# Performance work log

Measured on AMD Instinct MI355X. Metric: run time of the kernel, lower is better.

The kernel has to match this reference:

```python
import jax, jax.numpy as jnp
import numpy as np

EPS = 1e-5
TEMP = 2.0

def _dwconv(x, k, dil):
    # depthwise conv, NCHW, kernel OIHW with I=1, groups=C, 'same' padding
    p = dil
    return jax.lax.conv_general_dilated(
        x, k, window_strides=(1, 1), padding=[(p, p), (p, p)],
        rhs_dilation=(dil, dil),
        dimension_numbers=('NCHW', 'OIHW', 'NCHW'),
        feature_group_count=x.shape[1])

def _bn_gelu(y, g, b, m, v):
    scale = (g / jnp.sqrt(v + EPS))[None, :, None, None]
    z = (y - m[None, :, None, None]) * scale + b[None, :, None, None]
    return jax.nn.gelu(z, approximate=False)  # torch nn.GELU default = exact erf

def _pw(feat, w, b):
    # 1x1 pointwise conv with bias
    return jnp.einsum('oi,bihw->bohw', w, feat) + b[None, :, None, None]

def _forward(x, rw, rb,
             e0_k, e0_g, e0_b, e0_m, e0_v, e0_pw, e0_pb,
             e1_k, e1_g, e1_b, e1_m, e1_v, e1_pw, e1_pb,
             e2_k, e2_g, e2_b, e2_m, e2_v, e2_pw, e2_pb):
    # ---- global routing (eval mode: no noise) ----
    pooled = x.mean(axis=(2, 3))                    # [B, C]
    logits = pooled @ rw.T + rb                     # [B, 3]
    prob = jax.nn.softmax(logits / TEMP, axis=-1)
    tp, ti = jax.lax.top_k(prob, 1)                 # top_k = 1
    w = (tp / tp.sum(axis=-1, keepdims=True))[:, 0] # [B], == 1.0 for k=1
    idx = ti[:, 0]                                  # [B]

    # ---- heterogeneous experts, each over full batch, masked by weight ----
    f0 = _pw(_bn_gelu(_dwconv(x, e0_k, 1), e0_g, e0_b, e0_m, e0_v), e0_pw, e0_pb)
    f1 = _pw(_bn_gelu(_dwconv(x, e1_k, 2), e1_g, e1_b, e1_m, e1_v), e1_pw, e1_pb)
    f2 = _pw(_bn_gelu(jnp.einsum('oi,bihw->bohw', e2_k, x), e2_g, e2_b, e2_m, e2_v), e2_pw, e2_pb)

    out = jnp.zeros_like(x)
    for i, fi in enumerate((f0, f1, f2)):
        wi = jnp.where(idx == i, w, 0.0)[:, None, None, None]
        out = out + wi * fi
    return out

def setup_inputs() -> dict:
    key = jax.random.key(0)
    ks = jax.random.split(key, 24)
    B, C, H, W = 32, 256, 64, 64
    d = {
        'x': jax.random.normal(ks[0], (B, C, H, W), jnp.float32),
        'rw': jax.random.normal(ks[1], (3, C), jnp.float32) * 0.02,
        'rb': jnp.zeros((3,), jnp.float32),
    }
    kshapes = [(C, 1, 3, 3), (C, 1, 3, 3), (C, C)]
    for i in range(3):
        base = 2 + i * 4
        d[f'e{i}_k'] = jax.random.normal(ks[base], kshapes[i], jnp.float32) * 0.1
        d[f'e{i}_g'] = jnp.ones((C,), jnp.float32)
        d[f'e{i}_b'] = jnp.zeros((C,), jnp.float32)
        d[f'e{i}_m'] = jax.random.normal(ks[base + 1], (C,), jnp.float32) * 0.1
        d[f'e{i}_v'] = jax.random.uniform(ks[base + 2], (C,), jnp.float32, 0.5, 1.5)
        d[f'e{i}_pw'] = jax.random.normal(ks[base + 3], (C, C), jnp.float32) / np.sqrt(C)
        d[f'e{i}_pb'] = jnp.zeros((C,), jnp.float32)
    return d

def reference(x, rw, rb,
              e0_k, e0_g, e0_b, e0_m, e0_v, e0_pw, e0_pb,
              e1_k, e1_g, e1_b, e1_m, e1_v, e1_pw, e1_pb,
              e2_k, e2_g, e2_b, e2_m, e2_v, e2_pw, e2_pb):
    return _forward(x, rw, rb,
                    e0_k, e0_g, e0_b, e0_m, e0_v, e0_pw, e0_pb,
                    e1_k, e1_g, e1_b, e1_m, e1_v, e1_pw, e1_pb,
                    e2_k, e2_g, e2_b, e2_m, e2_v, e2_pw, e2_pb)
```

## Files before the change

kernel.cpp:

```cpp
#include <hip/hip_runtime.h>
#include <math.h>

#define C 256
#define H 64
#define W 64
#define B 32
#define HW (H*W)
#define EPS 1e-5f
#define LSTR2 256

typedef __attribute__((ext_vector_type(8))) short short8;
typedef __attribute__((ext_vector_type(4))) short short4v;
typedef __attribute__((ext_vector_type(4))) float f32x4;

__device__ __forceinline__ float gelu_exact(float z) {
    return 0.5f * z * (1.0f + erff(z * 0.70710678f));
}
__device__ __forceinline__ short f2bf(float f) {
    union { float f; unsigned u; } v; v.f = f;
    unsigned r = v.u + 0x7fffu + ((v.u >> 16) & 1u);
    return (short)(r >> 16);
}
__device__ __forceinline__ float bf2f(short s) {
    union { unsigned u; float f; } v; v.u = ((unsigned)(unsigned short)s) << 16;
    return v.f;
}
__device__ __forceinline__ int swz8(int w) {
    return (((w & 7) ^ ((w >> 3) & 7)) << 3);
}
__device__ __forceinline__ void swz_hb(int bx, int by, int& h, int& b) {
    int wg  = bx + (by << 6);
    int xcd = wg & 7, lin = wg >> 3;
    b = lin >> 3;
    int j = lin & 7;
    h = (((xcd + b) & 7) << 3) + j;
}

__global__ __launch_bounds__(256) void pool_kernel(const float* __restrict__ x,
                                                   float* __restrict__ pooled) {
    int bc = blockIdx.x;
    const float4* p4 = (const float4*)(x + (size_t)bc * HW);
    int t = threadIdx.x;
    float s = 0.f;
    for (int i = t; i < HW/4; i += 256) {
        float4 v = p4[i];
        s += v.x + v.y + v.z + v.w;
    }
    for (int off = 32; off > 0; off >>= 1) s += __shfl_down(s, off, 64);
    __shared__ float wsum[4];
    if ((t & 63) == 0) wsum[t >> 6] = s;
    __syncthreads();
    if (t == 0) pooled[bc] = (wsum[0]+wsum[1]+wsum[2]+wsum[3]) * (1.f/HW);
}

__global__ __launch_bounds__(256) void prep_kernel(
    const float* __restrict__ s0, const float* __restrict__ s1,
    const float* __restrict__ s2, const float* __restrict__ s3,
    const float* __restrict__ e0k, const float* __restrict__ e1k,
    const float* __restrict__ g0, const float* __restrict__ b0,
    const float* __restrict__ m0, const float* __restrict__ v0,
    const float* __restrict__ g1, const float* __restrict__ b1,
    const float* __restrict__ m1, const float* __restrict__ v1,
    const float* __restrict__ g2, const float* __restrict__ b2,
    const float* __restrict__ m2, const float* __restrict__ v2,
    const float* __restrict__ pooled, const float* __restrict__ rw,
    const float* __restrict__ rb, int* __restrict__ idx,
    short* __restrict__ apackAll, float* __restrict__ kf0, float* __restrict__ kf1,
    float* __restrict__ scAll, float* __restrict__ shAll)
{
    if (blockIdx.x < 192) {
        int gid = blockIdx.x * 256 + threadIdx.x;
        int mat = gid >> 13;
        int c   = gid & 8191;
        int lane = c & 63;
        int ktmt = c >> 6;
        int mt = ktmt & 15, kt = ktmt >> 4;
        int o  = mt*16 + (lane & 15);
        int ci = kt*32 + (lane >> 4)*8;
        const float* src = (mat == 0) ? s0 : (mat == 1) ? s1 :
                           (mat == 2 || mat == 4) ? s2 : s3;
        bool lo = (mat >= 4);
        const float* p = src + o*C + ci;
        short8 v;
#pragma unroll
        for (int j = 0; j < 8; ++j) {
            float f = p[j];
            short hj = f2bf(f);
            v[j] = lo ? f2bf(f - bf2f(hj)) : hj;
        }
        *(short8*)&apackAll[(size_t)gid * 8] = v;
    } else if (blockIdx.x == 192) {
        int t = threadIdx.x;
        {
            float s = g0[t] / sqrtf(v0[t] + EPS);
            scAll[t] = s; shAll[t] = b0[t] - m0[t]*s;
#pragma unroll
            for (int j = 0; j < 9; ++j) kf0[t*12+j] = e0k[t*9+j]*s;
            kf0[t*12+9] = 0.f; kf0[t*12+10] = 0.f; kf0[t*12+11] = 0.f;
        }
        {
            float s = g1[t] / sqrtf(v1[t] + EPS);
            scAll[C+t] = s; shAll[C+t] = b1[t] - m1[t]*s;
#pragma unroll
            for (int j = 0; j < 9; ++j) kf1[t*12+j] = e1k[t*9+j]*s;
            kf1[t*12+9] = 0.f; kf1[t*12+10] = 0.f; kf1[t*12+11] = 0.f;
        }
        {
            float s = g2[t] / sqrtf(v2[t] + EPS);
            scAll[2*C+t] = s; shAll[2*C+t] = b2[t] - m2[t]*s;
        }
    } else {
        int t = threadIdx.x;
        if (t < 192) {
            int e = t >> 6, lane = t & 63;
            __shared__ float lg[3*B];
            for (int b = 0; b < B; ++b) {
                const float* p = pooled + b*C;
                const float* w = rw + e*C;
                float s = 0.f;
#pragma unroll
                for (int i = 0; i < 4; ++i) s += p[lane + i*64] * w[lane + i*64];
                for (int off = 32; off > 0; off >>= 1) s += __shfl_down(s, off, 64);
                if (lane == 0) lg[b*3 + e] = s + rb[e];
            }
            __syncthreads();
            if (t < B) {
                float l0 = lg[t*3], l1 = lg[t*3+1], l2 = lg[t*3+2];
                int best = 0; float bv = l0;
                if (l1 > bv) { bv = l1; best = 1; }
                if (l2 > bv) { bv = l2; best = 2; }
                idx[t] = best;
            }
        } else {
            __syncthreads();
        }
    }
}

template<int DIL>
__device__ __forceinline__ void conv_rows_t(const float* __restrict__ x,
                                            const float* __restrict__ kf,
                                            const float* __restrict__ sh,
                                            short* __restrict__ lds,
                                            int b, int h, int t) {
    const int strip = t & 7;
    const int w0 = strip * 8;
    const int cib = t >> 3;
#pragma unroll 1
    for (int iter = 0; iter < 8; ++iter) {
        int ci = iter*32 + cib;
        const float* xpl = x + (size_t)(b*C + ci) * HW;
        float fr[3][16];
        bool rv[3];
#pragma unroll
        for (int ky = 0; ky < 3; ++ky) {
            int y = h + (ky - 1)*DIL;
            rv[ky] = ((unsigned)y < H);
            if (rv[ky]) {
                const float* row = xpl + y*W;
                float4 fa = (strip > 0) ? *(const float4*)(row + w0 - 4) : float4{0,0,0,0};
                float4 fb = *(const float4*)(row + w0);
                float4 fc = *(const float4*)(row + w0 + 4);
                float4 fd = (strip < 7) ? *(const float4*)(row + w0 + 8) : float4{0,0,0,0};
                fr[ky][0]=fa.x; fr[ky][1]=fa.y; fr[ky][2]=fa.z; fr[ky][3]=fa.w;
                fr[ky][4]=fb.x; fr[ky][5]=fb.y; fr[ky][6]=fb.z; fr[ky][7]=fb.w;
                fr[ky][8]=fc.x; fr[ky][9]=fc.y; fr[ky][10]=fc.z; fr[ky][11]=fc.w;
                fr[ky][12]=fd.x; fr[ky][13]=fd.y; fr[ky][14]=fd.z; fr[ky][15]=fd.w;
            }
        }
        float4 k0 = *(const float4*)(kf + ci*12);
        float4 k1v = *(const float4*)(kf + ci*12 + 4);
        float wk[9] = {k0.x,k0.y,k0.z,k0.w,k1v.x,k1v.y,k1v.z,k1v.w, kf[ci*12+8]};
        float acc8[8] = {0,0,0,0,0,0,0,0};
#pragma unroll
        for (int ky = 0; ky < 3; ++ky) {
            if (rv[ky]) {
#pragma unroll
                for (int kx = 0; kx < 3; ++kx) {
                    float wv = wk[ky*3+kx];
                    const int base = 4 + (kx - 1)*DIL;
#pragma unroll
                    for (int j = 0; j < 8; ++j) acc8[j] += wv * fr[ky][base + j];
                }
            }
        }
        float shv = sh[ci];
#pragma unroll
        for (int j = 0; j < 8; ++j) {
            int w = w0 + j;
            lds[w*LSTR2 + (ci ^ swz8(w))] = f2bf(gelu_exact(acc8[j] + shv));
        }
    }
}

__global__ __launch_bounds__(256) void kconv(
    const float* __restrict__ x, const int* __restrict__ idx,
    const float* __restrict__ kf0, const float* __restrict__ kf1,
    const float* __restrict__ shAll, const short* __restrict__ apackAll,
    const float* __restrict__ e0pb, const float* __restrict__ e1pb,
    float* __restrict__ out)
{
    __shared__ short lds[W*LSTR2];
    int h, b;
    swz_hb(blockIdx.x, blockIdx.y, h, b);
    const int e = idx[b];
    if (e >= 2) return;
    const int t = threadIdx.x;
    const int lane = t & 63, wid = t >> 6;
    const int l15 = lane & 15, quad = lane >> 4;

    if (e == 0) conv_rows_t<1>(x, kf0, shAll,     lds, b, h, t);
    else        conv_rows_t<2>(x, kf1, shAll + C, lds, b, h, t);
    __syncthreads();

    const short* pwf = apackAll + (size_t)e * 65536;
    f32x4 acc[4][4];
#pragma unroll
    for (int i = 0; i < 4; ++i)
#pragma unroll
        for (int wt = 0; wt < 4; ++wt) acc[i][wt] = (f32x4){0.f,0.f,0.f,0.f};
    for (int kt = 0; kt < 8; ++kt) {
        short8 bf[4];
#pragma unroll
        for (int wt = 0; wt < 4; ++wt) {
            int w = wt*16 + l15;
            bf[wt] = *(const short8*)&lds[w*LSTR2 + ((kt*32 + quad*8) ^ swz8(w))];
        }
        short8 af[4];
#pragma unroll
        for (int i = 0; i < 4; ++i)
            af[i] = *(const short8*)&pwf[((size_t)(kt*16 + wid*4 + i)*64 + lane)*8];
#pragma unroll
        for (int i = 0; i < 4; ++i)
#pragma unroll
            for (int wt = 0; wt < 4; ++wt)
                acc[i][wt] = __builtin_amdgcn_mfma_f32_16x16x32_bf16(
                    af[i], bf[wt], acc[i][wt], 0, 0, 0);
    }

    const float* pb = (e == 0) ? e0pb : e1pb;
#pragma unroll
    for (int i = 0; i < 4; ++i) {
        int ob = wid*64 + i*16 + quad*4;
        float4 p4 = *(const float4*)&pb[ob];
        float pbv[4] = {p4.x, p4.y, p4.z, p4.w};
#pragma unroll
        for (int wt = 0; wt < 4; ++wt) {
            int w = wt*16 + l15;
#pragma unroll
            for (int r = 0; r < 4; ++r)
                out[((size_t)(b*C + ob + r))*HW + h*W + w] = acc[i][wt][r] + pbv[r];
        }
    }
}

__device__ __forceinline__ void gemm3t(const short* __restrict__ aH,
                                       const short* __restrict__ aL,
                                       const short* __restrict__ ldsH,
                                       const short* __restrict__ ldsL,
                                       int lane, int wid, f32x4 acc[4][4])
{
    const int l15 = lane & 15, quad = lane >> 4;
    for (int kt = 0; kt < 8; ++kt) {
        short8 bH[4], bL[4];
#pragma unroll
        for (int wt = 0; wt < 4; ++wt) {
            int w = wt*16 + l15;
            int off = w*LSTR2 + ((kt*32 + quad*8) ^ swz8(w));
            bH[wt] = *(const short8*)&ldsH[off];
            bL[wt] = *(const short8*)&ldsL[off];
        }
        short8 fH[4], fL[4];
#pragma unroll
        for (int i = 0; i < 4; ++i) {
            size_t off = ((size_t)(kt*16 + wid*4 + i)*64 + lane)*8;
            fH[i] = *(const short8*)&aH[off];
            fL[i] = *(const short8*)&aL[off];
        }
#pragma unroll
        for (int i = 0; i < 4; ++i)
#pragma unroll
            for (int wt = 0; wt < 4; ++wt) {
                acc[i][wt] = __builtin_amdgcn_mfma_f32_16x16x32_bf16(fH[i], bH[wt], acc[i][wt], 0, 0, 0);
                acc[i][wt] = __builtin_amdgcn_mfma_f32_16x16x32_bf16(fH[i], bL[wt], acc[i][wt], 0, 0, 0);
                acc[i][wt] = __builtin_amdgcn_mfma_f32_16x16x32_bf16(fL[i], bH[wt], acc[i][wt], 0, 0, 0);
            }
    }
}

__global__ __launch_bounds__(256) void ke2(
    const float* __restrict__ x, const int* __restrict__ idx,
    const float* __restrict__ scAll, const float* __restrict__ shAll,
    const short* __restrict__ apackAll, const float* __restrict__ e2pb,
    float* __restrict__ out)
{
    __shared__ short ldsH[W*LSTR2];
    __shared__ short ldsL[W*LSTR2];
    int h, b;
    swz_hb(blockIdx.x, blockIdx.y, h, b);
    if (idx[b] != 2) return;
    const int t = threadIdx.x;
    const int lane = t & 63, wid = t >> 6;
    const int l15 = lane & 15, quad = lane >> 4;

    {
        const int w = t & 63;
        const int vsw = swz8(w);
        const int ci0w = wid * 64;
#pragma unroll 1
        for (int k = 0; k < 8; ++k) {
            int ci0 = ci0w + k*8;
            const float* px = x + ((size_t)(b*C + ci0)*H + h)*W + w;
            float f[8];
#pragma unroll
            for (int j = 0; j < 8; ++j) f[j] = px[(size_t)j * HW];
            short8 hi, lo;
#pragma unroll
            for (int j = 0; j < 8; ++j) {
                short hj = f2bf(f[j]);
                hi[j] = hj;
                lo[j] = f2bf(f[j] - bf2f(hj));
            }
            int col = ci0 ^ vsw;
            *(short8*)&ldsH[w*LSTR2 + col] = hi;
            *(short8*)&ldsL[w*LSTR2 + col] = lo;
        }
    }
    __syncthreads();

    f32x4 acc[4][4];
#pragma unroll
    for (int i = 0; i < 4; ++i)
#pragma unroll
        for (int wt = 0; wt < 4; ++wt) acc[i][wt] = (f32x4){0.f,0.f,0.f,0.f};
    gemm3t(apackAll + (size_t)3*65536, apackAll + (size_t)5*65536,
           ldsH, ldsL, lane, wid, acc);
    __syncthreads();

    {
        const float* sc2 = scAll + 2*C;
        const float* sh2 = shAll + 2*C;
#pragma unroll
        for (int i = 0; i < 4; ++i) {
            int cob = wid*64 + i*16 + quad*4;
            float4 s4 = *(const float4*)&sc2[cob];
            float4 h4 = *(const float4*)&sh2[cob];
            float ss[4] = {s4.x, s4.y, s4.z, s4.w};
            float hh[4] = {h4.x, h4.y, h4.z, h4.w};
#pragma unroll
            for (int wt = 0; wt < 4; ++wt) {
                int w = wt*16 + l15;
                int col = cob ^ swz8(w);
                short4v ph, pl;
#pragma unroll
                for (int r = 0; r < 4; ++r) {
                    float f = gelu_exact(acc[i][wt][r]*ss[r] + hh[r]);
                    short hj = f2bf(f);
                    ph[r] = hj;
                    pl[r] = f2bf(f - bf2f(hj));
                }
                *(short4v*)&ldsH[w*LSTR2 + col] = ph;
                *(short4v*)&ldsL[w*LSTR2 + col] = pl;
            }
        }
    }
    __syncthreads();

#pragma unroll
    for (int i = 0; i < 4; ++i)
#pragma unroll
        for (int wt = 0; wt < 4; ++wt) acc[i][wt] = (f32x4){0.f,0.f,0.f,0.f};
    gemm3t(apackAll + (size_t)2*65536, apackAll + (size_t)4*65536,
           ldsH, ldsL, lane, wid, acc);

#pragma unroll
    for (int i = 0; i < 4; ++i) {
        int ob = wid*64 + i*16 + quad*4;
        float4 p4 = *(const float4*)&e2pb[ob];
        float pbv[4] = {p4.x, p4.y, p4.z, p4.w};
#pragma unroll
        for (int wt = 0; wt < 4; ++wt) {
            int w = wt*16 + l15;
#pragma unroll
            for (int r = 0; r < 4; ++r)
                out[((size_t)(b*C + ob + r))*HW + h*W + w] = acc[i][wt][r] + pbv[r];
        }
    }
}

extern "C" void kernel_launch(void* const* d_in, const int* in_sizes, int n_in,
                              void* d_out, int out_size, void* d_ws, size_t ws_size,
                              hipStream_t stream) {
    const float* x    = (const float*)d_in[0];
    const float* rw   = (const float*)d_in[1];
    const float* rb   = (const float*)d_in[2];
    const float* e0k  = (const float*)d_in[3];
    const float* e0g  = (const float*)d_in[4];
    const float* e0b  = (const float*)d_in[5];
    const float* e0m  = (const float*)d_in[6];
    const float* e0v  = (const float*)d_in[7];
    const float* e0pw = (const float*)d_in[8];
    const float* e0pb = (const float*)d_in[9];
    const float* e1k  = (const float*)d_in[10];
    const float* e1g  = (const float*)d_in[11];
    const float* e1b  = (const float*)d_in[12];
    const float* e1m  = (const float*)d_in[13];
    const float* e1v  = (const float*)d_in[14];
    const float* e1pw = (const float*)d_in[15];
    const float* e1pb = (const float*)d_in[16];
    const float* e2k  = (const float*)d_in[17];
    const float* e2g  = (const float*)d_in[18];
    const float* e2b  = (const float*)d_in[19];
    const float* e2m  = (const float*)d_in[20];
    const float* e2v  = (const float*)d_in[21];
    const float* e2pw = (const float*)d_in[22];
    const float* e2pb = (const float*)d_in[23];
    float* out = (float*)d_out;

    char* wsb = (char*)d_ws;
    float* pooled   = (float*)wsb;
    int*   idx      = (int*)(wsb + 32768);
    float* scAll    = (float*)(wsb + 32896);
    float* shAll    = (float*)(wsb + 35968);
    float* kf0      = (float*)(wsb + 39040);
    float* kf1      = (float*)(wsb + 51328);
    short* apackAll = (short*)(wsb + 63616);

    pool_kernel<<<B*C, 256, 0, stream>>>(x, pooled);
    prep_kernel<<<194, 256, 0, stream>>>(e0pw, e1pw, e2pw, e2k, e0k, e1k,
                                         e0g, e0b, e0m, e0v,
                                         e1g, e1b, e1m, e1v,
                                         e2g, e2b, e2m, e2v,
                                         pooled, rw, rb, idx,
                                         apackAll, kf0, kf1, scAll, shAll);
    kconv<<<dim3(H, B), 256, 0, stream>>>(x, idx, kf0, kf1, shAll, apackAll,
                                          e0pb, e1pb, out);
    ke2<<<dim3(H, B), 256, 0, stream>>>(x, idx, scAll, shAll, apackAll,
                                        e2pb, out);
}
```

Measured before the change: 407.2 us.

## Merge conv and pointwise expert kernels into one launch with half-width e2 tiles

Replaces the separate kconv and ke2 kernels with a single kexp kernel that branches on the routed expert per batch. This removes one launch and the grid of early-exiting blocks. The expert-2 path now processes each row in two 32-column halves, so its hi/lo split buffers fit in the same 32 KB LDS array as the conv path. That lowers LDS per block and may raise occupancy, at the cost of more barriers and re-reading the weight fragments twice per row.

```diff
diff --git a/kernel.cpp b/kernel.cpp
--- a/kernel.cpp
+++ b/kernel.cpp
@@ -193,197 +193,188 @@
     }
 }
 
-__global__ __launch_bounds__(256) void kconv(
+template<int NWT>
+__device__ __forceinline__ void gemm3t(const short* __restrict__ aH,
+                                       const short* __restrict__ aL,
+                                       const short* __restrict__ ldsH,
+                                       const short* __restrict__ ldsL,
+                                       int lane, int wid, f32x4 acc[4][NWT])
+{
+    const int l15 = lane & 15, quad = lane >> 4;
+    for (int kt = 0; kt < 8; ++kt) {
+        short8 bH[NWT], bL[NWT];
+#pragma unroll
+        for (int wt = 0; wt < NWT; ++wt) {
+            int w = wt*16 + l15;
+            int off = w*LSTR2 + ((kt*32 + quad*8) ^ swz8(w));
+            bH[wt] = *(const short8*)&ldsH[off];
+            bL[wt] = *(const short8*)&ldsL[off];
+        }
+        short8 fH[4], fL[4];
+#pragma unroll
+        for (int i = 0; i < 4; ++i) {
+            size_t off = ((size_t)(kt*16 + wid*4 + i)*64 + lane)*8;
+            fH[i] = *(const short8*)&aH[off];
+            fL[i] = *(const short8*)&aL[off];
+        }
+#pragma unroll
+        for (int i = 0; i < 4; ++i)
+#pragma unroll
+            for (int wt = 0; wt < NWT; ++wt) {
+                acc[i][wt] = __builtin_amdgcn_mfma_f32_16x16x32_bf16(fH[i], bH[wt], acc[i][wt], 0, 0, 0);
+                acc[i][wt] = __builtin_amdgcn_mfma_f32_16x16x32_bf16(fH[i], bL[wt], acc[i][wt], 0, 0, 0);
+                acc[i][wt] = __builtin_amdgcn_mfma_f32_16x16x32_bf16(fL[i], bH[wt], acc[i][wt], 0, 0, 0);
+            }
+    }
+}
+
+__global__ __launch_bounds__(256) void kexp(
     const float* __restrict__ x, const int* __restrict__ idx,
     const float* __restrict__ kf0, const float* __restrict__ kf1,
-    const float* __restrict__ shAll, const short* __restrict__ apackAll,
+    const float* __restrict__ scAll, const float* __restrict__ shAll,
+    const short* __restrict__ apackAll,
     const float* __restrict__ e0pb, const float* __restrict__ e1pb,
+    const float* __restrict__ e2pb,
     float* __restrict__ out)
 {
     __shared__ short lds[W*LSTR2];
     int h, b;
     swz_hb(blockIdx.x, blockIdx.y, h, b);
     const int e = idx[b];
-    if (e >= 2) return;
     const int t = threadIdx.x;
     const int lane = t & 63, wid = t >> 6;
     const int l15 = lane & 15, quad = lane >> 4;
 
-    if (e == 0) conv_rows_t<1>(x, kf0, shAll,     lds, b, h, t);
-    else        conv_rows_t<2>(x, kf1, shAll + C, lds, b, h, t);
-    __syncthreads();
-
-    const short* pwf = apackAll + (size_t)e * 65536;
-    f32x4 acc[4][4];
-#pragma unroll
-    for (int i = 0; i < 4; ++i)
-#pragma unroll
-        for (int wt = 0; wt < 4; ++wt) acc[i][wt] = (f32x4){0.f,0.f,0.f,0.f};
-    for (int kt = 0; kt < 8; ++kt) {
-        short8 bf[4];
-#pragma unroll
-        for (int wt = 0; wt < 4; ++wt) {
-            int w = wt*16 + l15;
-            bf[wt] = *(const short8*)&lds[w*LSTR2 + ((kt*32 + quad*8) ^ swz8(w))];
-        }
-        short8 af[4];
+    if (e < 2) {
+        if (e == 0) conv_rows_t<1>(x, kf0, shAll,     lds, b, h, t);
+        else        conv_rows_t<2>(x, kf1, shAll + C, lds, b, h, t);
+        __syncthreads();
+
+        const short* pwf = apackAll + (size_t)e * 65536;
+        f32x4 acc[4][4];
 #pragma unroll
         for (int i = 0; i < 4; ++i)
-            af[i] = *(const short8*)&pwf[((size_t)(kt*16 + wid*4 + i)*64 + lane)*8];
-#pragma unroll
-        for (int i = 0; i < 4; ++i)
-#pragma unroll
-            for (int wt = 0; wt < 4; ++wt)
-                acc[i][wt] = __builtin_amdgcn_mfma_f32_16x16x32_bf16(
-                    af[i], bf[wt], acc[i][wt], 0, 0, 0);
-    }
-
-    const float* pb = (e == 0) ? e0pb : e1pb;
-#pragma unroll
-    for (int i = 0; i < 4; ++i) {
-        int ob = wid*64 + i*16 + quad*4;
-        float4 p4 = *(const float4*)&pb[ob];
-        float pbv[4] = {p4.x, p4.y, p4.z, p4.w};
-#pragma unroll
-        for (int wt = 0; wt < 4; ++wt) {
-            int w = wt*16 + l15;
-#pragma unroll
-            for (int r = 0; r < 4; ++r)
-                out[((size_t)(b*C + ob + r))*HW + h*W + w] = acc[i][wt][r] + pbv[r];
-        }
-    }
-}
-
-__device__ __forceinline__ void gemm3t(const short* __restrict__ aH,
-                                       const short* __restrict__ aL,
-                                       const short* __restrict__ ldsH,
-                                       const short* __restrict__ ldsL,
-                                       int lane, int wid, f32x4 acc[4][4])
-{
-    const int l15 = lane & 15, quad = lane >> 4;
-    for (int kt = 0; kt < 8; ++kt) {
-        short8 bH[4], bL[4];
-#pragma unroll
-        for (int wt = 0; wt < 4; ++wt) {
-            int w = wt*16 + l15;
-            int off = w*LSTR2 + ((kt*32 + quad*8) ^ swz8(w));
-            bH[wt] = *(const short8*)&ldsH[off];
-            bL[wt] = *(const short8*)&ldsL[off];
-        }
-        short8 fH[4], fL[4];
+#pragma unroll
+            for (int wt = 0; wt < 4; ++wt) acc[i][wt] = (f32x4){0.f,0.f,0.f,0.f};
+        for (int kt = 0; kt < 8; ++kt) {
+            short8 bf[4];
+#pragma unroll
+            for (int wt = 0; wt < 4; ++wt) {
+                int w = wt*16 + l15;
+                bf[wt] = *(const short8*)&lds[w*LSTR2 + ((kt*32 + quad*8) ^ swz8(w))];
+            }
+            short8 af[4];
+#pragma unroll
+            for (int i = 0; i < 4; ++i)
+                af[i] = *(const short8*)&pwf[((size_t)(kt*16 + wid*4 + i)*64 + lane)*8];
+#pragma unroll
+            for (int i = 0; i < 4; ++i)
+#pragma unroll
+                for (int wt = 0; wt < 4; ++wt)
+                    acc[i][wt] = __builtin_amdgcn_mfma_f32_16x16x32_bf16(
+                        af[i], bf[wt], acc[i][wt], 0, 0, 0);
+        }
+
+        const float* pb = (e == 0) ? e0pb : e1pb;
 #pragma unroll
         for (int i = 0; i < 4; ++i) {
-            size_t off = ((size_t)(kt*16 + wid*4 + i)*64 + lane)*8;
-            fH[i] = *(const short8*)&aH[off];
-            fL[i] = *(const short8*)&aL[off];
-        }
-#pragma unroll
-        for (int i = 0; i < 4; ++i)
+            int ob = wid*64 + i*16 + quad*4;
+            float4 p4 = *(const float4*)&pb[ob];
+            float pbv[4] = {p4.x, p4.y, p4.z, p4.w};
 #pragma unroll
             for (int wt = 0; wt < 4; ++wt) {
-                acc[i][wt] = __builtin_amdgcn_mfma_f32_16x16x32_bf16(fH[i], bH[wt], acc[i][wt], 0, 0, 0);
-                acc[i][wt] = __builtin_amdgcn_mfma_f32_16x16x32_bf16(fH[i], bL[wt], acc[i][wt], 0, 0, 0);
-                acc[i][wt] = __builtin_amdgcn_mfma_f32_16x16x32_bf16(fL[i], bH[wt], acc[i][wt], 0, 0, 0);
-            }
-    }
-}
-
-__global__ __launch_bounds__(256) void ke2(
-    const float* __restrict__ x, const int* __restrict__ idx,
-    const float* __restrict__ scAll, const float* __restrict__ shAll,
-    const short* __restrict__ apackAll, const float* __restrict__ e2pb,
-    float* __restrict__ out)
-{
-    __shared__ short ldsH[W*LSTR2];
-    __shared__ short ldsL[W*LSTR2];
-    int h, b;
-    swz_hb(blockIdx.x, blockIdx.y, h, b);
-    if (idx[b] != 2) return;
-    const int t = threadIdx.x;
-    const int lane = t & 63, wid = t >> 6;
-    const int l15 = lane & 15, quad = lane >> 4;
-
-    {
-        const int w = t & 63;
-        const int vsw = swz8(w);
-        const int ci0w = wid * 64;
-#pragma unroll 1
-        for (int k = 0; k < 8; ++k) {
-            int ci0 = ci0w + k*8;
-            const float* px = x + ((size_t)(b*C + ci0)*H + h)*W + w;
-            float f[8];
-#pragma unroll
-            for (int j = 0; j < 8; ++j) f[j] = px[(size_t)j * HW];
-            short8 hi, lo;
-#pragma unroll
-            for (int j = 0; j < 8; ++j) {
-                short hj = f2bf(f[j]);
-                hi[j] = hj;
-                lo[j] = f2bf(f[j] - bf2f(hj));
-            }
-            int col = ci0 ^ vsw;
-            *(short8*)&ldsH[w*LSTR2 + col] = hi;
-            *(short8*)&ldsL[w*LSTR2 + col] = lo;
-        }
-    }
-    __syncthreads();
-
-    f32x4 acc[4][4];
-#pragma unroll
-    for (int i = 0; i < 4; ++i)
-#pragma unroll
-        for (int wt = 0; wt < 4; ++wt) acc[i][wt] = (f32x4){0.f,0.f,0.f,0.f};
-    gemm3t(apackAll + (size_t)3*65536, apackAll + (size_t)5*65536,
-           ldsH, ldsL, lane, wid, acc);
-    __syncthreads();
-
-    {
+                int w = wt*16 + l15;
+#pragma unroll
+                for (int r = 0; r < 4; ++r)
+                    out[((size_t)(b*C + ob + r))*HW + h*W + w] = acc[i][wt][r] + pbv[r];
+            }
+        }
+    } else {
+        short* ldsH = lds;
+        short* ldsL = lds + 32*LSTR2;
         const float* sc2 = scAll + 2*C;
         const float* sh2 = shAll + 2*C;
-#pragma unroll
-        for (int i = 0; i < 4; ++i) {
-            int cob = wid*64 + i*16 + quad*4;
-            float4 s4 = *(const float4*)&sc2[cob];
-            float4 h4 = *(const float4*)&sh2[cob];
-            float ss[4] = {s4.x, s4.y, s4.z, s4.w};
-            float hh[4] = {h4.x, h4.y, h4.z, h4.w};
-#pragma unroll
-            for (int wt = 0; wt < 4; ++wt) {
-                int w = wt*16 + l15;
-                int col = cob ^ swz8(w);
-                short4v ph, pl;
-#pragma unroll
-                for (int r = 0; r < 4; ++r) {
-                    float f = gelu_exact(acc[i][wt][r]*ss[r] + hh[r]);
-                    short hj = f2bf(f);
-                    ph[r] = hj;
-                    pl[r] = f2bf(f - bf2f(hj));
+#pragma unroll 1
+        for (int hf = 0; hf < 2; ++hf) {
+            if (hf) __syncthreads();
+            {
+                const int wl = t & 31, g = t >> 5;
+                const int vsw = swz8(wl);
+#pragma unroll
+                for (int k = 0; k < 4; ++k) {
+                    int ci0 = g*32 + k*8;
+                    const float* px = x + ((size_t)(b*C + ci0)*H + h)*W + hf*32 + wl;
+                    float f[8];
+#pragma unroll
+                    for (int j = 0; j < 8; ++j) f[j] = px[(size_t)j * HW];
+                    short8 hi, lo;
+#pragma unroll
+                    for (int j = 0; j < 8; ++j) {
+                        short hj = f2bf(f[j]);
+                        hi[j] = hj;
+                        lo[j] = f2bf(f[j] - bf2f(hj));
+                    }
+                    int col = ci0 ^ vsw;
+                    *(short8*)&ldsH[wl*LSTR2 + col] = hi;
+                    *(short8*)&ldsL[wl*LSTR2 + col] = lo;
                 }
-                *(short4v*)&ldsH[w*LSTR2 + col] = ph;
-                *(short4v*)&ldsL[w*LSTR2 + col] = pl;
-            }
-        }
-    }
-    __syncthreads();
-
-#pragma unroll
-    for (int i = 0; i < 4; ++i)
-#pragma unroll
-        for (int wt = 0; wt < 4; ++wt) acc[i][wt] = (f32x4){0.f,0.f,0.f,0.f};
-    gemm3t(apackAll + (size_t)2*65536, apackAll + (size_t)4*65536,
-           ldsH, ldsL, lane, wid, acc);
-
-#pragma unroll
-    for (int i = 0; i < 4; ++i) {
-        int ob = wid*64 + i*16 + quad*4;
-        float4 p4 = *(const float4*)&e2pb[ob];
-        float pbv[4] = {p4.x, p4.y, p4.z, p4.w};
-#pragma unroll
-        for (int wt = 0; wt < 4; ++wt) {
-            int w = wt*16 + l15;
-#pragma unroll
-            for (int r = 0; r < 4; ++r)
-                out[((size_t)(b*C + ob + r))*HW + h*W + w] = acc[i][wt][r] + pbv[r];
+            }
+            __syncthreads();
+
+            f32x4 acc[4][2];
+#pragma unroll
+            for (int i = 0; i < 4; ++i)
+#pragma unroll
+                for (int wt = 0; wt < 2; ++wt) acc[i][wt] = (f32x4){0.f,0.f,0.f,0.f};
+            gemm3t<2>(apackAll + (size_t)3*65536, apackAll + (size_t)5*65536,
+                      ldsH, ldsL, lane, wid, acc);
+            __syncthreads();
+
+#pragma unroll
+            for (int i = 0; i < 4; ++i) {
+                int cob = wid*64 + i*16 + quad*4;
+                float4 s4 = *(const float4*)&sc2[cob];
+                float4 h4 = *(const float4*)&sh2[cob];
+                float ss[4] = {s4.x, s4.y, s4.z, s4.w};
+                float hh[4] = {h4.x, h4.y, h4.z, h4.w};
+#pragma unroll
+                for (int wt = 0; wt < 2; ++wt) {
+                    int w = wt*16 + l15;
+                    int col = cob ^ swz8(w);
+                    short4v ph, pl;
+#pragma unroll
+                    for (int r = 0; r < 4; ++r) {
+                        float f = gelu_exact(acc[i][wt][r]*ss[r] + hh[r]);
+                        short hj = f2bf(f);
+                        ph[r] = hj;
+                        pl[r] = f2bf(f - bf2f(hj));
+                    }
+                    *(short4v*)&ldsH[w*LSTR2 + col] = ph;
+                    *(short4v*)&ldsL[w*LSTR2 + col] = pl;
+                }
+            }
+            __syncthreads();
+
+#pragma unroll
+            for (int i = 0; i < 4; ++i)
+#pragma unroll
+                for (int wt = 0; wt < 2; ++wt) acc[i][wt] = (f32x4){0.f,0.f,0.f,0.f};
+            gemm3t<2>(apackAll + (size_t)2*65536, apackAll + (size_t)4*65536,
+                      ldsH, ldsL, lane, wid, acc);
+
+#pragma unroll
+            for (int i = 0; i < 4; ++i) {
+                int ob = wid*64 + i*16 + quad*4;
+                float4 p4 = *(const float4*)&e2pb[ob];
+                float pbv[4] = {p4.x, p4.y, p4.z, p4.w};
+#pragma unroll
+                for (int wt = 0; wt < 2; ++wt) {
+                    int w = hf*32 + wt*16 + l15;
+#pragma unroll
+                    for (int r = 0; r < 4; ++r)
+                        out[((size_t)(b*C + ob + r))*HW + h*W + w] = acc[i][wt][r] + pbv[r];
+                }
+            }
         }
     }
 }
@@ -433,8 +424,6 @@
                                          e2g, e2b, e2m, e2v,
                                          pooled, rw, rb, idx,
                                          apackAll, kf0, kf1, scAll, shAll);
-    kconv<<<dim3(H, B), 256, 0, stream>>>(x, idx, kf0, kf1, shAll, apackAll,
-                                          e0pb, e1pb, out);
-    ke2<<<dim3(H, B), 256, 0, stream>>>(x, idx, scAll, shAll, apackAll,
-                                        e2pb, out);
-}
+    kexp<<<dim3(H, B), 256, 0, stream>>>(x, idx, kf0, kf1, scAll, shAll,
+                                         apackAll, e0pb, e1pb, e2pb, out);
+}
```

Result: slower. 512.6 us (+25.9%).
